# Optimization experiments

Measured on AMD Instinct MI355X. Metric: run time of the kernel, lower is better.

The kernel has to match this reference:

```python
import jax, jax.numpy as jnp
import numpy as np

N_NODES = 102400
N_EDGES = 1638400
DIMS = [128, 64, 32, 1]  # decoder_dim=128, decoder_l=3, last layer -> 1


def setup_inputs() -> dict:
    key = jax.random.key(0)
    ks = jax.random.split(key, 10)
    inp = {
        'b_z': jax.random.normal(ks[0], (N_NODES, DIMS[0]), jnp.float32),
        'src': jax.random.randint(ks[1], (N_EDGES,), 0, N_NODES, jnp.int64 if jax.config.jax_enable_x64 else jnp.int32),
        'dst': jax.random.randint(ks[2], (N_EDGES,), 0, N_NODES, jnp.int64 if jax.config.jax_enable_x64 else jnp.int32),
        'edge_weight': jax.random.uniform(ks[3], (N_EDGES,), jnp.float32),
        'b_size': 100,
    }
    # GraphConv weights: W [in, out], bias [out] (DGL xavier init; randn ok for ref)
    for i in range(3):
        inp[f'W{i}'] = jax.random.normal(ks[4 + i], (DIMS[i], DIMS[i + 1]), jnp.float32) * (1.0 / np.sqrt(DIMS[i]))
        inp[f'b{i}'] = jnp.zeros((DIMS[i + 1],), jnp.float32)
    return inp


def _gcn_layer(h, src, dst, ew, W, b, activate):
    n = h.shape[0]
    ones = jnp.ones((src.shape[0],), h.dtype)
    # norm='both': symmetric degree normalization with plain (unweighted) degrees
    out_deg = jnp.clip(jax.ops.segment_sum(ones, src, num_segments=n), 1.0)
    in_deg = jnp.clip(jax.ops.segment_sum(ones, dst, num_segments=n), 1.0)
    h = h * (out_deg ** -0.5)[:, None]
    h = h @ W  # in_feats > out_feats: transform before aggregation (DGL order)
    msg = h[src] * ew[:, None]           # [E, out] edge-weighted gather
    agg = jax.ops.segment_sum(msg, dst, num_segments=n)  # scatter-add
    agg = agg * (in_deg ** -0.5)[:, None] + b
    return jnp.tanh(agg) if activate else agg


def reference(b_z, src, dst, edge_weight, b_size, W0, b0, W1, b1, W2, b2):
    h = b_z
    h = _gcn_layer(h, src, dst, edge_weight, W0, b0, True)
    h = _gcn_layer(h, src, dst, edge_weight, W1, b1, True)
    h = _gcn_layer(h, src, dst, edge_weight, W2, b2, False)
    return h.reshape(b_size, -1)
```

## Files before the change

### kernel.cpp

```cpp
#include <hip/hip_runtime.h>
#include <hip/hip_fp16.h>
#include <math.h>

#define N_NODES 102400
#define N_EDGES 1638400
#define NB 100
#define PB 256
#define EPB (N_EDGES/PB)

union H4 { int2 i2; __half h[4]; };

__global__ __launch_bounds__(256) void histA_kernel(const int* __restrict__ src, const int* __restrict__ dst,
                                                    int* __restrict__ histD, int* __restrict__ histS) {
    __shared__ int hD[NB], hS[NB];
    int tid = threadIdx.x;
    if (tid < NB) { hD[tid] = 0; hS[tid] = 0; }
    __syncthreads();
    int base = blockIdx.x * EPB;
    for (int i = tid; i < EPB; i += 256) {
        atomicAdd(&hD[dst[base + i] >> 10], 1);
        atomicAdd(&hS[src[base + i] >> 10], 1);
    }
    __syncthreads();
    if (tid < NB) {
        histD[blockIdx.x * NB + tid] = hD[tid];
        histS[blockIdx.x * NB + tid] = hS[tid];
    }
}

__global__ __launch_bounds__(256) void scanB_kernel(const int* __restrict__ histD, const int* __restrict__ histS,
                                                    int* __restrict__ offD, int* __restrict__ offS,
                                                    int* __restrict__ coarseD, int* __restrict__ coarseS) {
    __shared__ int totD[NB], totS[NB], baseD[NB + 1], baseS[NB + 1];
    int t = threadIdx.x;
    if (t < NB) { int s = 0; for (int k = 0; k < PB; k++) s += histD[k * NB + t]; totD[t] = s; }
    else if (t >= 128 && t < 128 + NB) { int j = t - 128; int s = 0; for (int k = 0; k < PB; k++) s += histS[k * NB + j]; totS[j] = s; }
    __syncthreads();
    if (t == 0)   { int r = 0; for (int j = 0; j < NB; j++) { baseD[j] = r; r += totD[j]; } baseD[NB] = r; }
    if (t == 128) { int r = 0; for (int j = 0; j < NB; j++) { baseS[j] = r; r += totS[j]; } baseS[NB] = r; }
    __syncthreads();
    if (t < NB) { int r = baseD[t]; for (int k = 0; k < PB; k++) { offD[k * NB + t] = r; r += histD[k * NB + t]; } }
    else if (t >= 128 && t < 128 + NB) { int j = t - 128; int r = baseS[j]; for (int k = 0; k < PB; k++) { offS[k * NB + j] = r; r += histS[k * NB + j]; } }
    if (t <= NB) coarseD[t] = baseD[t];
    if (t >= 128 && t <= 128 + NB) coarseS[t - 128] = baseS[t - 128];
}

__global__ __launch_bounds__(256) void partC_kernel(const int* __restrict__ src, const int* __restrict__ dst,
                                                    const float* __restrict__ ew,
                                                    const int* __restrict__ offD, const int* __restrict__ offS,
                                                    int2* __restrict__ partD, int* __restrict__ partS) {
    __shared__ int cD[NB], cS[NB];
    int tid = threadIdx.x;
    if (tid < NB) { cD[tid] = offD[blockIdx.x * NB + tid]; cS[tid] = offS[blockIdx.x * NB + tid]; }
    __syncthreads();
    int base = blockIdx.x * EPB;
    for (int i = tid; i < EPB; i += 256) {
        int s = src[base + i], d = dst[base + i];
        float w = ew[base + i];
        int p = atomicAdd(&cD[d >> 10], 1);
        partD[p] = make_int2(s | ((d & 1023) << 17), __float_as_int(w));
        int q = atomicAdd(&cS[s >> 10], 1);
        partS[q] = s & 1023;
    }
}

__global__ __launch_bounds__(1024) void fineS_kernel(const int* __restrict__ partS, const int* __restrict__ coarseS,
                                                     float* __restrict__ outdeg_inv) {
    __shared__ int hist[1024];
    int tid = threadIdx.x;
    hist[tid] = 0;
    __syncthreads();
    int beg = coarseS[blockIdx.x], end = coarseS[blockIdx.x + 1];
    for (int i = beg + tid; i < end; i += 1024) atomicAdd(&hist[partS[i]], 1);
    __syncthreads();
    outdeg_inv[blockIdx.x * 1024 + tid] = 1.0f / sqrtf((float)max(hist[tid], 1));
}

__global__ __launch_bounds__(1024) void fineD_kernel(const int2* __restrict__ partD, const int* __restrict__ coarseD,
                                                     const float* __restrict__ outdeg_inv,
                                                     int2* __restrict__ edge_perm, int* __restrict__ row_off,
                                                     float* __restrict__ indeg_inv) {
    __shared__ int hist[1024], cursor[1024];
    __shared__ int wsum[16];
    int tid = threadIdx.x, lane = tid & 63, wid = tid >> 6;
    hist[tid] = 0;
    __syncthreads();
    int beg = coarseD[blockIdx.x], end = coarseD[blockIdx.x + 1];
    for (int i = beg + tid; i < end; i += 1024) atomicAdd(&hist[(partD[i].x >> 17) & 1023], 1);
    __syncthreads();
    int v = hist[tid];
    int x = v;
    #pragma unroll
    for (int s = 1; s < 64; s <<= 1) { int t = __shfl_up(x, s, 64); if (lane >= s) x += t; }
    if (lane == 63) wsum[wid] = x;
    __syncthreads();
    if (wid == 0) {
        int ws = (lane < 16) ? wsum[lane] : 0;
        int y = ws;
        #pragma unroll
        for (int s = 1; s < 16; s <<= 1) { int t = __shfl_up(y, s, 64); if (lane >= s) y += t; }
        if (lane < 16) wsum[lane] = y - ws;
    }
    __syncthreads();
    int ex = wsum[wid] + x - v;
    cursor[tid] = beg + ex;
    int node = blockIdx.x * 1024 + tid;
    row_off[node] = beg + ex;
    indeg_inv[node] = 1.0f / sqrtf((float)max(v, 1));
    if (blockIdx.x == NB - 1 && tid == 0) row_off[N_NODES] = N_EDGES;
    __syncthreads();
    for (int i = beg + tid; i < end; i += 1024) {
        int2 t2 = partD[i];
        int d = (t2.x >> 17) & 1023, s = t2.x & 0x1FFFF;
        int p = atomicAdd(&cursor[d], 1);
        float w = __int_as_float(t2.y) * outdeg_inv[s];
        edge_perm[p] = make_int2(s, __float_as_int(w));
    }
}

template<int K, int C, int RN>
__global__ __launch_bounds__(256) void gemm_tile_kernel(
    const float* __restrict__ h, const float* __restrict__ W, __half* __restrict__ out) {
    constexpr int BM = 64;
    constexpr int RM = 4;
    constexpr int KC = 64;
    constexpr int TX = C / RN;
    constexpr int TY = BM / RM;
    static_assert(TX * TY == 256, "bad tile");
    static_assert(RN == 4, "fp16 epilogue assumes RN==4");

    __shared__ float Ws[K * C];
    __shared__ float Hs[KC][BM + 4];

    const int tid = threadIdx.x;
    const long brow = (long)blockIdx.x * BM;

    for (int i = tid; i < K * C; i += 256) Ws[i] = W[i];

    const int tx = tid % TX;
    const int ty = tid / TX;
    float acc[RM][RN] = {};

    const int lr = tid % 16;
    const int lk = tid / 16;

    for (int kc = 0; kc < K; kc += KC) {
        __syncthreads();
        #pragma unroll
        for (int p0 = 0; p0 < BM; p0 += 16) {
            const int r = p0 + lr;
            const float4 hv = *(const float4*)(h + (brow + r) * K + kc + lk * 4);
            Hs[lk * 4 + 0][r] = hv.x;
            Hs[lk * 4 + 1][r] = hv.y;
            Hs[lk * 4 + 2][r] = hv.z;
            Hs[lk * 4 + 3][r] = hv.w;
        }
        __syncthreads();

        #pragma unroll
        for (int k = 0; k < KC; ++k) {
            const float4 a4 = *(const float4*)&Hs[k][ty * RM];
            const float av[RM] = {a4.x, a4.y, a4.z, a4.w};
            float b[RN];
            *(float4*)b = *(const float4*)&Ws[(kc + k) * C + tx * RN];
            #pragma unroll
            for (int i = 0; i < RM; ++i)
                #pragma unroll
                for (int j = 0; j < RN; ++j)
                    acc[i][j] += av[i] * b[j];
        }
    }

    #pragma unroll
    for (int i = 0; i < RM; ++i) {
        const long row = brow + ty * RM + i;
        __half2 p01 = __floats2half2_rn(acc[i][0], acc[i][1]);
        __half2 p23 = __floats2half2_rn(acc[i][2], acc[i][3]);
        int2 packed = make_int2(*(int*)&p01, *(int*)&p23);
        *(int2*)(out + row * C + tx * RN) = packed;
    }
}

__global__ __launch_bounds__(256) void agg64_gemm_kernel(
    const __half* __restrict__ ht, const int* __restrict__ row_off,
    const int2* __restrict__ ep, const float* __restrict__ indeg_inv,
    const float* __restrict__ b0, const float* __restrict__ W1,
    __half* __restrict__ ht1, int N) {
    __shared__ float W1s[64 * 32];
    __shared__ float h1s[4][64];
    int tid = threadIdx.x;
    {
        const float4* W1v = (const float4*)W1;
        float4* W1sv = (float4*)W1s;
        W1sv[tid] = W1v[tid];
        W1sv[tid + 256] = W1v[tid + 256];
    }
    __syncthreads();

    int wave = (blockIdx.x * blockDim.x + tid) >> 6;
    int lane = tid & 63;
    if (wave >= N) return;
    int chunk = lane & 15;
    int eslot = lane >> 4;
    int beg = row_off[wave], end = row_off[wave + 1];
    const char* htb = (const char*)ht;
    unsigned coff = (unsigned)(chunk << 3);

    float4 a0 = {0, 0, 0, 0}, a1 = {0, 0, 0, 0};
    for (int e = beg; e < end; e += 8) {
        int ei0 = e + eslot, ei1 = e + 4 + eslot;
        int2 d0 = ep[min(ei0, end - 1)];
        int2 d1 = ep[min(ei1, end - 1)];
        float w0 = (ei0 < end) ? __int_as_float(d0.y) : 0.0f;
        float w1 = (ei1 < end) ? __int_as_float(d1.y) : 0.0f;
        H4 r0, r1;
        r0.i2 = *(const int2*)(htb + (((unsigned)d0.x << 7) | coff));
        r1.i2 = *(const int2*)(htb + (((unsigned)d1.x << 7) | coff));
        a0.x = fmaf(__half2float(r0.h[0]), w0, a0.x);
        a0.y = fmaf(__half2float(r0.h[1]), w0, a0.y);
        a0.z = fmaf(__half2float(r0.h[2]), w0, a0.z);
        a0.w = fmaf(__half2float(r0.h[3]), w0, a0.w);
        a1.x = fmaf(__half2float(r1.h[0]), w1, a1.x);
        a1.y = fmaf(__half2float(r1.h[1]), w1, a1.y);
        a1.z = fmaf(__half2float(r1.h[2]), w1, a1.z);
        a1.w = fmaf(__half2float(r1.h[3]), w1, a1.w);
    }
    a0.x += a1.x; a0.y += a1.y; a0.z += a1.z; a0.w += a1.w;
    #pragma unroll
    for (int s = 16; s <= 32; s <<= 1) {
        a0.x += __shfl_xor(a0.x, s, 64);
        a0.y += __shfl_xor(a0.y, s, 64);
        a0.z += __shfl_xor(a0.z, s, 64);
        a0.w += __shfl_xor(a0.w, s, 64);
    }
    int wv = tid >> 6;
    if (eslot == 0) {
        float sc = indeg_inv[wave];
        float4 b = *(const float4*)(b0 + chunk * 4);
        float4 v;
        v.x = tanhf(a0.x * sc + b.x);
        v.y = tanhf(a0.y * sc + b.y);
        v.z = tanhf(a0.z * sc + b.z);
        v.w = tanhf(a0.w * sc + b.w);
        *(float4*)&h1s[wv][chunk * 4] = v;
    }
    int c = lane & 31, half = lane >> 5;
    float t = 0.0f;
    #pragma unroll
    for (int j4 = 0; j4 < 8; ++j4) {
        int k = half * 32 + j4 * 4;
        float4 hh = *(const float4*)&h1s[wv][k];
        t += hh.x * W1s[(k + 0) * 32 + c];
        t += hh.y * W1s[(k + 1) * 32 + c];
        t += hh.z * W1s[(k + 2) * 32 + c];
        t += hh.w * W1s[(k + 3) * 32 + c];
    }
    t += __shfl_xor(t, 32, 64);
    if (half == 0) ht1[(long)wave * 32 + c] = __float2half_rn(t);
}

__global__ void agg32_dot_kernel(const __half* __restrict__ ht, const int* __restrict__ row_off,
                                 const int2* __restrict__ ep,
                                 const float* __restrict__ indeg_inv, const float* __restrict__ bias,
                                 const float* __restrict__ W2, float* __restrict__ ht2, int N) {
    int wave = (blockIdx.x * blockDim.x + threadIdx.x) >> 6;
    int lane = threadIdx.x & 63;
    if (wave >= N) return;
    int chunk = lane & 7;
    int eslot = lane >> 3;
    int beg = row_off[wave], end = row_off[wave + 1];
    const char* htb = (const char*)ht;
    unsigned coff = (unsigned)(chunk << 3);
    float4 a0 = {0, 0, 0, 0}, a1 = {0, 0, 0, 0};
    for (int e = beg; e < end; e += 16) {
        int ei0 = e + eslot, ei1 = e + 8 + eslot;
        int2 d0 = ep[min(ei0, end - 1)];
        int2 d1 = ep[min(ei1, end - 1)];
        float w0 = (ei0 < end) ? __int_as_float(d0.y) : 0.0f;
        float w1 = (ei1 < end) ? __int_as_float(d1.y) : 0.0f;
        H4 r0, r1;
        r0.i2 = *(const int2*)(htb + (((unsigned)d0.x << 6) | coff));
        r1.i2 = *(const int2*)(htb + (((unsigned)d1.x << 6) | coff));
        a0.x = fmaf(__half2float(r0.h[0]), w0, a0.x);
        a0.y = fmaf(__half2float(r0.h[1]), w0, a0.y);
        a0.z = fmaf(__half2float(r0.h[2]), w0, a0.z);
        a0.w = fmaf(__half2float(r0.h[3]), w0, a0.w);
        a1.x = fmaf(__half2float(r1.h[0]), w1, a1.x);
        a1.y = fmaf(__half2float(r1.h[1]), w1, a1.y);
        a1.z = fmaf(__half2float(r1.h[2]), w1, a1.z);
        a1.w = fmaf(__half2float(r1.h[3]), w1, a1.w);
    }
    a0.x += a1.x; a0.y += a1.y; a0.z += a1.z; a0.w += a1.w;
    #pragma unroll
    for (int s = 8; s <= 32; s <<= 1) {
        a0.x += __shfl_xor(a0.x, s, 64);
        a0.y += __shfl_xor(a0.y, s, 64);
        a0.z += __shfl_xor(a0.z, s, 64);
        a0.w += __shfl_xor(a0.w, s, 64);
    }
    float sc = indeg_inv[wave];
    float4 b = *(const float4*)(bias + chunk * 4);
    float4 w2 = *(const float4*)(W2 + chunk * 4);
    float t = tanhf(a0.x * sc + b.x) * w2.x
            + tanhf(a0.y * sc + b.y) * w2.y
            + tanhf(a0.z * sc + b.z) * w2.z
            + tanhf(a0.w * sc + b.w) * w2.w;
    t += __shfl_xor(t, 1, 64);
    t += __shfl_xor(t, 2, 64);
    t += __shfl_xor(t, 4, 64);
    if (lane == 0) ht2[wave] = t;
}

__global__ void agg1_kernel(const float* __restrict__ ht2, const int* __restrict__ row_off,
                            const int2* __restrict__ ep,
                            const float* __restrict__ indeg_inv, const float* __restrict__ bias,
                            float* __restrict__ out, int N) {
    int wave = (blockIdx.x * blockDim.x + threadIdx.x) >> 6;
    int lane = threadIdx.x & 63;
    int sub = lane >> 4;
    int slot = lane & 15;
    int node = wave * 4 + sub;
    if (node >= N) return;
    int beg = row_off[node], end = row_off[node + 1];
    float acc = 0.0f;
    for (int e = beg + slot; e < end; e += 16) {
        int2 t = ep[e];
        acc += ht2[t.x] * __int_as_float(t.y);
    }
    #pragma unroll
    for (int s = 1; s <= 8; s <<= 1) acc += __shfl_xor(acc, s, 64);
    if (slot == 0) out[node] = acc * indeg_inv[node] + bias[0];
}

extern "C" void kernel_launch(void* const* d_in, const int* in_sizes, int n_in,
                              void* d_out, int out_size, void* d_ws, size_t ws_size,
                              hipStream_t stream) {
    const float* b_z = (const float*)d_in[0];
    const int*   src = (const int*)d_in[1];
    const int*   dst = (const int*)d_in[2];
    const float* ew  = (const float*)d_in[3];
    const float* W0 = (const float*)d_in[5];
    const float* b0 = (const float*)d_in[6];
    const float* W1 = (const float*)d_in[7];
    const float* b1 = (const float*)d_in[8];
    const float* W2 = (const float*)d_in[9];
    const float* b2 = (const float*)d_in[10];
    float* out = (float*)d_out;

    const int N = N_NODES;
    const int E = N_EDGES;

    char* p = (char*)d_ws;
    int*   row_off    = (int*)p;            p += (size_t)(N + 4) * 4;
    float* outdeg_inv = (float*)p;          p += (size_t)N * 4;
    float* indeg_inv  = (float*)p;          p += (size_t)N * 4;
    int*   histD      = (int*)p;            p += (size_t)PB * NB * 4;
    int*   histS      = (int*)p;            p += (size_t)PB * NB * 4;
    int*   offD       = (int*)p;            p += (size_t)PB * NB * 4;
    int*   offS       = (int*)p;            p += (size_t)PB * NB * 4;
    int*   coarseD    = (int*)p;            p += (size_t)(NB + 4) * 4;
    int*   coarseS    = (int*)p;            p += (size_t)(NB + 4) * 4;
    int2*  edge_perm  = (int2*)p;           p += (size_t)E * 8;
    float* bufA       = (float*)p;          p += (size_t)N * 64 * 4;
    float* bufB       = (float*)p;
    int2*   partD = (int2*)bufA;
    int*    partS = (int*)bufB;
    __half* ht    = (__half*)bufA;
    __half* ht1   = (__half*)bufB;
    float*  ht2   = bufA;

    histA_kernel<<<PB, 256, 0, stream>>>(src, dst, histD, histS);
    scanB_kernel<<<1, 256, 0, stream>>>(histD, histS, offD, offS, coarseD, coarseS);
    partC_kernel<<<PB, 256, 0, stream>>>(src, dst, ew, offD, offS, partD, partS);
    fineS_kernel<<<NB, 1024, 0, stream>>>(partS, coarseS, outdeg_inv);
    fineD_kernel<<<NB, 1024, 0, stream>>>(partD, coarseD, outdeg_inv, edge_perm, row_off, indeg_inv);

    gemm_tile_kernel<128, 64, 4><<<N / 64, 256, 0, stream>>>(b_z, W0, ht);

    agg64_gemm_kernel<<<N / 4, 256, 0, stream>>>(ht, row_off, edge_perm, indeg_inv, b0, W1, ht1, N);

    agg32_dot_kernel<<<N / 4, 256, 0, stream>>>(ht1, row_off, edge_perm, indeg_inv, b1, W2, ht2, N);

    agg1_kernel<<<N / 16, 256, 0, stream>>>(ht2, row_off, edge_perm, indeg_inv, b2, out, N);
}
```

Baseline: 338.9 us.

## Merge build and aggregation kernels into persistent kernels with grid barriers

The five CSR-build kernels become one persistent kernel, and the three aggregation layers become another. Both use software grid barriers built on atomic counters, and the aggregation kernel runs grid-stride loops over nodes. The fine-histogram stages now run with 256 threads instead of 1024 and handle four nodes per thread. This is meant to remove launch gaps and tail effects between many small dependent kernels. In exchange, every block must be co-resident or the barriers deadlock, and barrier spinning plus lower parallelism in the fine stages add cost.

```diff
diff --git a/kernel.cpp b/kernel.cpp
--- a/kernel.cpp
+++ b/kernel.cpp
@@ -7,114 +7,140 @@
 #define NB 100
 #define PB 256
 #define EPB (N_EDGES/PB)
+#define AGG_BLOCKS 1536
+#define AGG_WAVES (AGG_BLOCKS*4)
 
 union H4 { int2 i2; __half h[4]; };
 
-__global__ __launch_bounds__(256) void histA_kernel(const int* __restrict__ src, const int* __restrict__ dst,
-                                                    int* __restrict__ histD, int* __restrict__ histS) {
+__device__ __forceinline__ void grid_sync(int* bar, int idx, int nblocks) {
+    __syncthreads();
+    if (threadIdx.x == 0) {
+        __threadfence();
+        __hip_atomic_fetch_add(&bar[idx], 1, __ATOMIC_RELEASE, __HIP_MEMORY_SCOPE_AGENT);
+        while (__hip_atomic_load(&bar[idx], __ATOMIC_ACQUIRE, __HIP_MEMORY_SCOPE_AGENT) < nblocks)
+            __builtin_amdgcn_s_sleep(2);
+        __threadfence();
+    }
+    __syncthreads();
+}
+
+__global__ __launch_bounds__(256) void mega_build_kernel(
+    const int* __restrict__ src, const int* __restrict__ dst, const float* __restrict__ ew,
+    int* __restrict__ histD, int* __restrict__ histS,
+    int* __restrict__ offD, int* __restrict__ offS,
+    int* __restrict__ coarseD, int* __restrict__ coarseS,
+    int2* __restrict__ partD, int* __restrict__ partS,
+    int2* __restrict__ edge_perm, int* __restrict__ row_off,
+    float* __restrict__ outdeg_inv, float* __restrict__ indeg_inv,
+    int* __restrict__ bar) {
     __shared__ int hD[NB], hS[NB];
-    int tid = threadIdx.x;
+    __shared__ int hist_f[1024];
+    __shared__ int cur_f[1024];
+    __shared__ int wsum[4];
+    const int tid = threadIdx.x;
+    const int bid = blockIdx.x;
+    const int lane = tid & 63, wid = tid >> 6;
+
     if (tid < NB) { hD[tid] = 0; hS[tid] = 0; }
     __syncthreads();
-    int base = blockIdx.x * EPB;
-    for (int i = tid; i < EPB; i += 256) {
-        atomicAdd(&hD[dst[base + i] >> 10], 1);
-        atomicAdd(&hS[src[base + i] >> 10], 1);
+    {
+        int base = bid * EPB;
+        for (int i = tid; i < EPB; i += 256) {
+            atomicAdd(&hD[dst[base + i] >> 10], 1);
+            atomicAdd(&hS[src[base + i] >> 10], 1);
+        }
     }
     __syncthreads();
     if (tid < NB) {
-        histD[blockIdx.x * NB + tid] = hD[tid];
-        histS[blockIdx.x * NB + tid] = hS[tid];
-    }
-}
-
-__global__ __launch_bounds__(256) void scanB_kernel(const int* __restrict__ histD, const int* __restrict__ histS,
-                                                    int* __restrict__ offD, int* __restrict__ offS,
-                                                    int* __restrict__ coarseD, int* __restrict__ coarseS) {
-    __shared__ int totD[NB], totS[NB], baseD[NB + 1], baseS[NB + 1];
-    int t = threadIdx.x;
-    if (t < NB) { int s = 0; for (int k = 0; k < PB; k++) s += histD[k * NB + t]; totD[t] = s; }
-    else if (t >= 128 && t < 128 + NB) { int j = t - 128; int s = 0; for (int k = 0; k < PB; k++) s += histS[k * NB + j]; totS[j] = s; }
-    __syncthreads();
-    if (t == 0)   { int r = 0; for (int j = 0; j < NB; j++) { baseD[j] = r; r += totD[j]; } baseD[NB] = r; }
-    if (t == 128) { int r = 0; for (int j = 0; j < NB; j++) { baseS[j] = r; r += totS[j]; } baseS[NB] = r; }
-    __syncthreads();
-    if (t < NB) { int r = baseD[t]; for (int k = 0; k < PB; k++) { offD[k * NB + t] = r; r += histD[k * NB + t]; } }
-    else if (t >= 128 && t < 128 + NB) { int j = t - 128; int r = baseS[j]; for (int k = 0; k < PB; k++) { offS[k * NB + j] = r; r += histS[k * NB + j]; } }
-    if (t <= NB) coarseD[t] = baseD[t];
-    if (t >= 128 && t <= 128 + NB) coarseS[t - 128] = baseS[t - 128];
-}
-
-__global__ __launch_bounds__(256) void partC_kernel(const int* __restrict__ src, const int* __restrict__ dst,
-                                                    const float* __restrict__ ew,
-                                                    const int* __restrict__ offD, const int* __restrict__ offS,
-                                                    int2* __restrict__ partD, int* __restrict__ partS) {
-    __shared__ int cD[NB], cS[NB];
-    int tid = threadIdx.x;
-    if (tid < NB) { cD[tid] = offD[blockIdx.x * NB + tid]; cS[tid] = offS[blockIdx.x * NB + tid]; }
-    __syncthreads();
-    int base = blockIdx.x * EPB;
-    for (int i = tid; i < EPB; i += 256) {
-        int s = src[base + i], d = dst[base + i];
-        float w = ew[base + i];
-        int p = atomicAdd(&cD[d >> 10], 1);
-        partD[p] = make_int2(s | ((d & 1023) << 17), __float_as_int(w));
-        int q = atomicAdd(&cS[s >> 10], 1);
-        partS[q] = s & 1023;
-    }
-}
-
-__global__ __launch_bounds__(1024) void fineS_kernel(const int* __restrict__ partS, const int* __restrict__ coarseS,
-                                                     float* __restrict__ outdeg_inv) {
-    __shared__ int hist[1024];
-    int tid = threadIdx.x;
-    hist[tid] = 0;
-    __syncthreads();
-    int beg = coarseS[blockIdx.x], end = coarseS[blockIdx.x + 1];
-    for (int i = beg + tid; i < end; i += 1024) atomicAdd(&hist[partS[i]], 1);
-    __syncthreads();
-    outdeg_inv[blockIdx.x * 1024 + tid] = 1.0f / sqrtf((float)max(hist[tid], 1));
-}
-
-__global__ __launch_bounds__(1024) void fineD_kernel(const int2* __restrict__ partD, const int* __restrict__ coarseD,
-                                                     const float* __restrict__ outdeg_inv,
-                                                     int2* __restrict__ edge_perm, int* __restrict__ row_off,
-                                                     float* __restrict__ indeg_inv) {
-    __shared__ int hist[1024], cursor[1024];
-    __shared__ int wsum[16];
-    int tid = threadIdx.x, lane = tid & 63, wid = tid >> 6;
-    hist[tid] = 0;
-    __syncthreads();
-    int beg = coarseD[blockIdx.x], end = coarseD[blockIdx.x + 1];
-    for (int i = beg + tid; i < end; i += 1024) atomicAdd(&hist[(partD[i].x >> 17) & 1023], 1);
-    __syncthreads();
-    int v = hist[tid];
-    int x = v;
-    #pragma unroll
-    for (int s = 1; s < 64; s <<= 1) { int t = __shfl_up(x, s, 64); if (lane >= s) x += t; }
-    if (lane == 63) wsum[wid] = x;
-    __syncthreads();
-    if (wid == 0) {
-        int ws = (lane < 16) ? wsum[lane] : 0;
-        int y = ws;
+        histD[bid * NB + tid] = hD[tid];
+        histS[bid * NB + tid] = hS[tid];
+    }
+    grid_sync(bar, 0, PB);
+
+    if (bid == 0) {
+        __shared__ int totD[NB], totS[NB], baseD[NB + 1], baseS[NB + 1];
+        int t = tid;
+        if (t < NB) { int s = 0; for (int k = 0; k < PB; k++) s += histD[k * NB + t]; totD[t] = s; }
+        else if (t >= 128 && t < 128 + NB) { int j = t - 128; int s = 0; for (int k = 0; k < PB; k++) s += histS[k * NB + j]; totS[j] = s; }
+        __syncthreads();
+        if (t == 0)   { int r = 0; for (int j = 0; j < NB; j++) { baseD[j] = r; r += totD[j]; } baseD[NB] = r; }
+        if (t == 128) { int r = 0; for (int j = 0; j < NB; j++) { baseS[j] = r; r += totS[j]; } baseS[NB] = r; }
+        __syncthreads();
+        if (t < NB) { int r = baseD[t]; for (int k = 0; k < PB; k++) { offD[k * NB + t] = r; r += histD[k * NB + t]; } }
+        else if (t >= 128 && t < 128 + NB) { int j = t - 128; int r = baseS[j]; for (int k = 0; k < PB; k++) { offS[k * NB + j] = r; r += histS[k * NB + j]; } }
+        if (t <= NB) coarseD[t] = baseD[t];
+        if (t >= 128 && t <= 128 + NB) coarseS[t - 128] = baseS[t - 128];
+    }
+    grid_sync(bar, 1, PB);
+
+    if (tid < NB) { hD[tid] = offD[bid * NB + tid]; hS[tid] = offS[bid * NB + tid]; }
+    __syncthreads();
+    {
+        int base = bid * EPB;
+        for (int i = tid; i < EPB; i += 256) {
+            int s = src[base + i], d = dst[base + i];
+            float w = ew[base + i];
+            int p = atomicAdd(&hD[d >> 10], 1);
+            partD[p] = make_int2(s | ((d & 1023) << 17), __float_as_int(w));
+            int q = atomicAdd(&hS[s >> 10], 1);
+            partS[q] = s & 1023;
+        }
+    }
+    grid_sync(bar, 2, PB);
+
+    if (bid < NB) {
         #pragma unroll
-        for (int s = 1; s < 16; s <<= 1) { int t = __shfl_up(y, s, 64); if (lane >= s) y += t; }
-        if (lane < 16) wsum[lane] = y - ws;
-    }
-    __syncthreads();
-    int ex = wsum[wid] + x - v;
-    cursor[tid] = beg + ex;
-    int node = blockIdx.x * 1024 + tid;
-    row_off[node] = beg + ex;
-    indeg_inv[node] = 1.0f / sqrtf((float)max(v, 1));
-    if (blockIdx.x == NB - 1 && tid == 0) row_off[N_NODES] = N_EDGES;
-    __syncthreads();
-    for (int i = beg + tid; i < end; i += 1024) {
-        int2 t2 = partD[i];
-        int d = (t2.x >> 17) & 1023, s = t2.x & 0x1FFFF;
-        int p = atomicAdd(&cursor[d], 1);
-        float w = __int_as_float(t2.y) * outdeg_inv[s];
-        edge_perm[p] = make_int2(s, __float_as_int(w));
+        for (int j = 0; j < 4; ++j) hist_f[tid + j * 256] = 0;
+        __syncthreads();
+        int beg = coarseS[bid], end = coarseS[bid + 1];
+        for (int i = beg + tid; i < end; i += 256) atomicAdd(&hist_f[partS[i]], 1);
+        __syncthreads();
+        int4 h = *(const int4*)&hist_f[tid * 4];
+        float4 o;
+        o.x = 1.0f / sqrtf((float)max(h.x, 1));
+        o.y = 1.0f / sqrtf((float)max(h.y, 1));
+        o.z = 1.0f / sqrtf((float)max(h.z, 1));
+        o.w = 1.0f / sqrtf((float)max(h.w, 1));
+        *(float4*)(outdeg_inv + bid * 1024 + tid * 4) = o;
+    }
+    grid_sync(bar, 3, PB);
+
+    if (bid < NB) {
+        #pragma unroll
+        for (int j = 0; j < 4; ++j) hist_f[tid + j * 256] = 0;
+        __syncthreads();
+        int beg = coarseD[bid], end = coarseD[bid + 1];
+        for (int i = beg + tid; i < end; i += 256) atomicAdd(&hist_f[(partD[i].x >> 17) & 1023], 1);
+        __syncthreads();
+        int4 h = *(const int4*)&hist_f[tid * 4];
+        int v = h.x + h.y + h.z + h.w;
+        int x = v;
+        #pragma unroll
+        for (int s = 1; s < 64; s <<= 1) { int t = __shfl_up(x, s, 64); if (lane >= s) x += t; }
+        if (lane == 63) wsum[wid] = x;
+        __syncthreads();
+        if (tid == 0) { int r = 0; for (int j = 0; j < 4; ++j) { int t = wsum[j]; wsum[j] = r; r += t; } }
+        __syncthreads();
+        int s0 = beg + wsum[wid] + x - v;
+        int s1 = s0 + h.x, s2 = s1 + h.y, s3 = s2 + h.z;
+        int node = bid * 1024 + tid * 4;
+        *(int4*)(row_off + node) = make_int4(s0, s1, s2, s3);
+        float4 ii;
+        ii.x = 1.0f / sqrtf((float)max(h.x, 1));
+        ii.y = 1.0f / sqrtf((float)max(h.y, 1));
+        ii.z = 1.0f / sqrtf((float)max(h.z, 1));
+        ii.w = 1.0f / sqrtf((float)max(h.w, 1));
+        *(float4*)(indeg_inv + node) = ii;
+        *(int4*)&cur_f[tid * 4] = make_int4(s0, s1, s2, s3);
+        if (bid == NB - 1 && tid == 0) row_off[N_NODES] = N_EDGES;
+        __syncthreads();
+        for (int i = beg + tid; i < end; i += 256) {
+            int2 t2 = partD[i];
+            int d = (t2.x >> 17) & 1023, s = t2.x & 0x1FFFF;
+            int p = atomicAdd(&cur_f[d], 1);
+            float w = __int_as_float(t2.y) * outdeg_inv[s];
+            edge_perm[p] = make_int2(s, __float_as_int(w));
+        }
     }
 }
 
@@ -181,14 +207,17 @@
     }
 }
 
-__global__ __launch_bounds__(256) void agg64_gemm_kernel(
+__global__ __launch_bounds__(256, 6) void mega_agg_kernel(
     const __half* __restrict__ ht, const int* __restrict__ row_off,
     const int2* __restrict__ ep, const float* __restrict__ indeg_inv,
     const float* __restrict__ b0, const float* __restrict__ W1,
-    __half* __restrict__ ht1, int N) {
+    __half* __restrict__ ht1,
+    const float* __restrict__ b1, const float* __restrict__ W2, float* __restrict__ ht2,
+    const float* __restrict__ b2, float* __restrict__ out,
+    int* __restrict__ bar) {
     __shared__ float W1s[64 * 32];
     __shared__ float h1s[4][64];
-    int tid = threadIdx.x;
+    const int tid = threadIdx.x;
     {
         const float4* W1v = (const float4*)W1;
         float4* W1sv = (float4*)W1s;
@@ -197,139 +226,136 @@
     }
     __syncthreads();
 
-    int wave = (blockIdx.x * blockDim.x + tid) >> 6;
-    int lane = tid & 63;
-    if (wave >= N) return;
-    int chunk = lane & 15;
-    int eslot = lane >> 4;
-    int beg = row_off[wave], end = row_off[wave + 1];
-    const char* htb = (const char*)ht;
-    unsigned coff = (unsigned)(chunk << 3);
-
-    float4 a0 = {0, 0, 0, 0}, a1 = {0, 0, 0, 0};
-    for (int e = beg; e < end; e += 8) {
-        int ei0 = e + eslot, ei1 = e + 4 + eslot;
-        int2 d0 = ep[min(ei0, end - 1)];
-        int2 d1 = ep[min(ei1, end - 1)];
-        float w0 = (ei0 < end) ? __int_as_float(d0.y) : 0.0f;
-        float w1 = (ei1 < end) ? __int_as_float(d1.y) : 0.0f;
-        H4 r0, r1;
-        r0.i2 = *(const int2*)(htb + (((unsigned)d0.x << 7) | coff));
-        r1.i2 = *(const int2*)(htb + (((unsigned)d1.x << 7) | coff));
-        a0.x = fmaf(__half2float(r0.h[0]), w0, a0.x);
-        a0.y = fmaf(__half2float(r0.h[1]), w0, a0.y);
-        a0.z = fmaf(__half2float(r0.h[2]), w0, a0.z);
-        a0.w = fmaf(__half2float(r0.h[3]), w0, a0.w);
-        a1.x = fmaf(__half2float(r1.h[0]), w1, a1.x);
-        a1.y = fmaf(__half2float(r1.h[1]), w1, a1.y);
-        a1.z = fmaf(__half2float(r1.h[2]), w1, a1.z);
-        a1.w = fmaf(__half2float(r1.h[3]), w1, a1.w);
-    }
-    a0.x += a1.x; a0.y += a1.y; a0.z += a1.z; a0.w += a1.w;
-    #pragma unroll
-    for (int s = 16; s <= 32; s <<= 1) {
-        a0.x += __shfl_xor(a0.x, s, 64);
-        a0.y += __shfl_xor(a0.y, s, 64);
-        a0.z += __shfl_xor(a0.z, s, 64);
-        a0.w += __shfl_xor(a0.w, s, 64);
-    }
-    int wv = tid >> 6;
-    if (eslot == 0) {
-        float sc = indeg_inv[wave];
-        float4 b = *(const float4*)(b0 + chunk * 4);
-        float4 v;
-        v.x = tanhf(a0.x * sc + b.x);
-        v.y = tanhf(a0.y * sc + b.y);
-        v.z = tanhf(a0.z * sc + b.z);
-        v.w = tanhf(a0.w * sc + b.w);
-        *(float4*)&h1s[wv][chunk * 4] = v;
-    }
-    int c = lane & 31, half = lane >> 5;
-    float t = 0.0f;
-    #pragma unroll
-    for (int j4 = 0; j4 < 8; ++j4) {
-        int k = half * 32 + j4 * 4;
-        float4 hh = *(const float4*)&h1s[wv][k];
-        t += hh.x * W1s[(k + 0) * 32 + c];
-        t += hh.y * W1s[(k + 1) * 32 + c];
-        t += hh.z * W1s[(k + 2) * 32 + c];
-        t += hh.w * W1s[(k + 3) * 32 + c];
-    }
-    t += __shfl_xor(t, 32, 64);
-    if (half == 0) ht1[(long)wave * 32 + c] = __float2half_rn(t);
-}
-
-__global__ void agg32_dot_kernel(const __half* __restrict__ ht, const int* __restrict__ row_off,
-                                 const int2* __restrict__ ep,
-                                 const float* __restrict__ indeg_inv, const float* __restrict__ bias,
-                                 const float* __restrict__ W2, float* __restrict__ ht2, int N) {
-    int wave = (blockIdx.x * blockDim.x + threadIdx.x) >> 6;
-    int lane = threadIdx.x & 63;
-    if (wave >= N) return;
-    int chunk = lane & 7;
-    int eslot = lane >> 3;
-    int beg = row_off[wave], end = row_off[wave + 1];
-    const char* htb = (const char*)ht;
-    unsigned coff = (unsigned)(chunk << 3);
-    float4 a0 = {0, 0, 0, 0}, a1 = {0, 0, 0, 0};
-    for (int e = beg; e < end; e += 16) {
-        int ei0 = e + eslot, ei1 = e + 8 + eslot;
-        int2 d0 = ep[min(ei0, end - 1)];
-        int2 d1 = ep[min(ei1, end - 1)];
-        float w0 = (ei0 < end) ? __int_as_float(d0.y) : 0.0f;
-        float w1 = (ei1 < end) ? __int_as_float(d1.y) : 0.0f;
-        H4 r0, r1;
-        r0.i2 = *(const int2*)(htb + (((unsigned)d0.x << 6) | coff));
-        r1.i2 = *(const int2*)(htb + (((unsigned)d1.x << 6) | coff));
-        a0.x = fmaf(__half2float(r0.h[0]), w0, a0.x);
-        a0.y = fmaf(__half2float(r0.h[1]), w0, a0.y);
-        a0.z = fmaf(__half2float(r0.h[2]), w0, a0.z);
-        a0.w = fmaf(__half2float(r0.h[3]), w0, a0.w);
-        a1.x = fmaf(__half2float(r1.h[0]), w1, a1.x);
-        a1.y = fmaf(__half2float(r1.h[1]), w1, a1.y);
-        a1.z = fmaf(__half2float(r1.h[2]), w1, a1.z);
-        a1.w = fmaf(__half2float(r1.h[3]), w1, a1.w);
-    }
-    a0.x += a1.x; a0.y += a1.y; a0.z += a1.z; a0.w += a1.w;
-    #pragma unroll
-    for (int s = 8; s <= 32; s <<= 1) {
-        a0.x += __shfl_xor(a0.x, s, 64);
-        a0.y += __shfl_xor(a0.y, s, 64);
-        a0.z += __shfl_xor(a0.z, s, 64);
-        a0.w += __shfl_xor(a0.w, s, 64);
-    }
-    float sc = indeg_inv[wave];
-    float4 b = *(const float4*)(bias + chunk * 4);
-    float4 w2 = *(const float4*)(W2 + chunk * 4);
-    float t = tanhf(a0.x * sc + b.x) * w2.x
-            + tanhf(a0.y * sc + b.y) * w2.y
-            + tanhf(a0.z * sc + b.z) * w2.z
-            + tanhf(a0.w * sc + b.w) * w2.w;
-    t += __shfl_xor(t, 1, 64);
-    t += __shfl_xor(t, 2, 64);
-    t += __shfl_xor(t, 4, 64);
-    if (lane == 0) ht2[wave] = t;
-}
-
-__global__ void agg1_kernel(const float* __restrict__ ht2, const int* __restrict__ row_off,
-                            const int2* __restrict__ ep,
-                            const float* __restrict__ indeg_inv, const float* __restrict__ bias,
-                            float* __restrict__ out, int N) {
-    int wave = (blockIdx.x * blockDim.x + threadIdx.x) >> 6;
-    int lane = threadIdx.x & 63;
-    int sub = lane >> 4;
-    int slot = lane & 15;
-    int node = wave * 4 + sub;
-    if (node >= N) return;
-    int beg = row_off[node], end = row_off[node + 1];
-    float acc = 0.0f;
-    for (int e = beg + slot; e < end; e += 16) {
-        int2 t = ep[e];
-        acc += ht2[t.x] * __int_as_float(t.y);
-    }
-    #pragma unroll
-    for (int s = 1; s <= 8; s <<= 1) acc += __shfl_xor(acc, s, 64);
-    if (slot == 0) out[node] = acc * indeg_inv[node] + bias[0];
+    const int lane = tid & 63;
+    const int wv = tid >> 6;
+    const int w = blockIdx.x * 4 + wv;
+
+    {
+        int chunk = lane & 15;
+        int eslot = lane >> 4;
+        const char* htb = (const char*)ht;
+        unsigned coff = (unsigned)(chunk << 3);
+        int c = lane & 31, half = lane >> 5;
+        for (int node = w; node < N_NODES; node += AGG_WAVES) {
+            int beg = row_off[node], end = row_off[node + 1];
+            float4 a0 = {0, 0, 0, 0}, a1 = {0, 0, 0, 0};
+            for (int e = beg; e < end; e += 8) {
+                int ei0 = e + eslot, ei1 = e + 4 + eslot;
+                int2 d0 = ep[min(ei0, end - 1)];
+                int2 d1 = ep[min(ei1, end - 1)];
+                float w0 = (ei0 < end) ? __int_as_float(d0.y) : 0.0f;
+                float w1 = (ei1 < end) ? __int_as_float(d1.y) : 0.0f;
+                H4 r0, r1;
+                r0.i2 = *(const int2*)(htb + (((unsigned)d0.x << 7) | coff));
+                r1.i2 = *(const int2*)(htb + (((unsigned)d1.x << 7) | coff));
+                a0.x = fmaf(__half2float(r0.h[0]), w0, a0.x);
+                a0.y = fmaf(__half2float(r0.h[1]), w0, a0.y);
+                a0.z = fmaf(__half2float(r0.h[2]), w0, a0.z);
+                a0.w = fmaf(__half2float(r0.h[3]), w0, a0.w);
+                a1.x = fmaf(__half2float(r1.h[0]), w1, a1.x);
+                a1.y = fmaf(__half2float(r1.h[1]), w1, a1.y);
+                a1.z = fmaf(__half2float(r1.h[2]), w1, a1.z);
+                a1.w = fmaf(__half2float(r1.h[3]), w1, a1.w);
+            }
+            a0.x += a1.x; a0.y += a1.y; a0.z += a1.z; a0.w += a1.w;
+            #pragma unroll
+            for (int s = 16; s <= 32; s <<= 1) {
+                a0.x += __shfl_xor(a0.x, s, 64);
+                a0.y += __shfl_xor(a0.y, s, 64);
+                a0.z += __shfl_xor(a0.z, s, 64);
+                a0.w += __shfl_xor(a0.w, s, 64);
+            }
+            if (eslot == 0) {
+                float sc = indeg_inv[node];
+                float4 b = *(const float4*)(b0 + chunk * 4);
+                float4 v;
+                v.x = tanhf(a0.x * sc + b.x);
+                v.y = tanhf(a0.y * sc + b.y);
+                v.z = tanhf(a0.z * sc + b.z);
+                v.w = tanhf(a0.w * sc + b.w);
+                *(float4*)&h1s[wv][chunk * 4] = v;
+            }
+            float t = 0.0f;
+            #pragma unroll
+            for (int j4 = 0; j4 < 8; ++j4) {
+                int k = half * 32 + j4 * 4;
+                float4 hh = *(const float4*)&h1s[wv][k];
+                t += hh.x * W1s[(k + 0) * 32 + c];
+                t += hh.y * W1s[(k + 1) * 32 + c];
+                t += hh.z * W1s[(k + 2) * 32 + c];
+                t += hh.w * W1s[(k + 3) * 32 + c];
+            }
+            t += __shfl_xor(t, 32, 64);
+            if (half == 0) ht1[(long)node * 32 + c] = __float2half_rn(t);
+        }
+    }
+    grid_sync(bar + 4, 0, AGG_BLOCKS);
+
+    {
+        int chunk = lane & 7;
+        int eslot = lane >> 3;
+        const char* htb = (const char*)ht1;
+        unsigned coff = (unsigned)(chunk << 3);
+        float4 b = *(const float4*)(b1 + chunk * 4);
+        float4 w2 = *(const float4*)(W2 + chunk * 4);
+        for (int node = w; node < N_NODES; node += AGG_WAVES) {
+            int beg = row_off[node], end = row_off[node + 1];
+            float4 a0 = {0, 0, 0, 0}, a1 = {0, 0, 0, 0};
+            for (int e = beg; e < end; e += 16) {
+                int ei0 = e + eslot, ei1 = e + 8 + eslot;
+                int2 d0 = ep[min(ei0, end - 1)];
+                int2 d1 = ep[min(ei1, end - 1)];
+                float w0 = (ei0 < end) ? __int_as_float(d0.y) : 0.0f;
+                float w1 = (ei1 < end) ? __int_as_float(d1.y) : 0.0f;
+                H4 r0, r1;
+                r0.i2 = *(const int2*)(htb + (((unsigned)d0.x << 6) | coff));
+                r1.i2 = *(const int2*)(htb + (((unsigned)d1.x << 6) | coff));
+                a0.x = fmaf(__half2float(r0.h[0]), w0, a0.x);
+                a0.y = fmaf(__half2float(r0.h[1]), w0, a0.y);
+                a0.z = fmaf(__half2float(r0.h[2]), w0, a0.z);
+                a0.w = fmaf(__half2float(r0.h[3]), w0, a0.w);
+                a1.x = fmaf(__half2float(r1.h[0]), w1, a1.x);
+                a1.y = fmaf(__half2float(r1.h[1]), w1, a1.y);
+                a1.z = fmaf(__half2float(r1.h[2]), w1, a1.z);
+                a1.w = fmaf(__half2float(r1.h[3]), w1, a1.w);
+            }
+            a0.x += a1.x; a0.y += a1.y; a0.z += a1.z; a0.w += a1.w;
+            #pragma unroll
+            for (int s = 8; s <= 32; s <<= 1) {
+                a0.x += __shfl_xor(a0.x, s, 64);
+                a0.y += __shfl_xor(a0.y, s, 64);
+                a0.z += __shfl_xor(a0.z, s, 64);
+                a0.w += __shfl_xor(a0.w, s, 64);
+            }
+            float sc = indeg_inv[node];
+            float t = tanhf(a0.x * sc + b.x) * w2.x
+                    + tanhf(a0.y * sc + b.y) * w2.y
+                    + tanhf(a0.z * sc + b.z) * w2.z
+                    + tanhf(a0.w * sc + b.w) * w2.w;
+            t += __shfl_xor(t, 1, 64);
+            t += __shfl_xor(t, 2, 64);
+            t += __shfl_xor(t, 4, 64);
+            if (lane == 0) ht2[node] = t;
+        }
+    }
+    grid_sync(bar + 4, 1, AGG_BLOCKS);
+
+    {
+        int sub = lane >> 4;
+        int slot = lane & 15;
+        float bb = b2[0];
+        for (int node = w * 4 + sub; node < N_NODES; node += AGG_WAVES * 4) {
+            int beg = row_off[node], end = row_off[node + 1];
+            float acc = 0.0f;
+            for (int e = beg + slot; e < end; e += 16) {
+                int2 t = ep[e];
+                acc += ht2[t.x] * __int_as_float(t.y);
+            }
+            #pragma unroll
+            for (int s = 1; s <= 8; s <<= 1) acc += __shfl_xor(acc, s, 64);
+            if (slot == 0) out[node] = acc * indeg_inv[node] + bb;
+        }
+    }
 }
 
 extern "C" void kernel_launch(void* const* d_in, const int* in_sizes, int n_in,
@@ -351,6 +377,7 @@
     const int E = N_EDGES;
 
     char* p = (char*)d_ws;
+    int*   bar        = (int*)p;            p += 64;
     int*   row_off    = (int*)p;            p += (size_t)(N + 4) * 4;
     float* outdeg_inv = (float*)p;          p += (size_t)N * 4;
     float* indeg_inv  = (float*)p;          p += (size_t)N * 4;
@@ -369,17 +396,14 @@
     __half* ht1   = (__half*)bufB;
     float*  ht2   = bufA;
 
-    histA_kernel<<<PB, 256, 0, stream>>>(src, dst, histD, histS);
-    scanB_kernel<<<1, 256, 0, stream>>>(histD, histS, offD, offS, coarseD, coarseS);
-    partC_kernel<<<PB, 256, 0, stream>>>(src, dst, ew, offD, offS, partD, partS);
-    fineS_kernel<<<NB, 1024, 0, stream>>>(partS, coarseS, outdeg_inv);
-    fineD_kernel<<<NB, 1024, 0, stream>>>(partD, coarseD, outdeg_inv, edge_perm, row_off, indeg_inv);
+    hipMemsetAsync(bar, 0, 64, stream);
+
+    mega_build_kernel<<<PB, 256, 0, stream>>>(src, dst, ew, histD, histS, offD, offS,
+                                              coarseD, coarseS, partD, partS,
+                                              edge_perm, row_off, outdeg_inv, indeg_inv, bar);
 
     gemm_tile_kernel<128, 64, 4><<<N / 64, 256, 0, stream>>>(b_z, W0, ht);
 
-    agg64_gemm_kernel<<<N / 4, 256, 0, stream>>>(ht, row_off, edge_perm, indeg_inv, b0, W1, ht1, N);
-
-    agg32_dot_kernel<<<N / 4, 256, 0, stream>>>(ht1, row_off, edge_perm, indeg_inv, b1, W2, ht2, N);
-
-    agg1_kernel<<<N / 16, 256, 0, stream>>>(ht2, row_off, edge_perm, indeg_inv, b2, out, N);
+    mega_agg_kernel<<<AGG_BLOCKS, 256, 0, stream>>>(ht, row_off, edge_perm, indeg_inv,
+                                                    b0, W1, ht1, b1, W2, ht2, b2, out, bar);
 }
```

After: 1.163 ms. 243% more time.
